# Optimization experiments

Hardware: AMD Instinct MI355X
Metric: run time of the kernel (lower is better)

The kernel has to match this reference:

```python
import jax, jax.numpy as jnp
import numpy as np

NDIM = 1024
NHEAD = 16
HEAD_DIM = NDIM // NHEAD


def setup_inputs() -> dict:
    key = jax.random.key(0)
    ks = jax.random.split(key, 12)
    B, L, C = 2, 2048, NDIM
    s = 0.02
    return {
        "q": jax.random.normal(ks[0], (B, L, C), jnp.float32),
        "k": jax.random.normal(ks[1], (B, L, C), jnp.float32),
        "v": jax.random.normal(ks[2], (B, L, C), jnp.float32),
        "Wq": jax.random.normal(ks[3], (C, C), jnp.float32) * s,
        "bq": jax.random.normal(ks[4], (C,), jnp.float32) * s,
        "Wk": jax.random.normal(ks[5], (C, C), jnp.float32) * s,
        "bk": jax.random.normal(ks[6], (C,), jnp.float32) * s,
        "Wv": jax.random.normal(ks[7], (C, C), jnp.float32) * s,
        "bv": jax.random.normal(ks[8], (C,), jnp.float32) * s,
        "Wo": jax.random.normal(ks[9], (C, C), jnp.float32) * s,
        "bo": jax.random.normal(ks[10], (C,), jnp.float32) * s,
    }


def reference(q, k, v, Wq, bq, Wk, bk, Wv, bv, Wo, bo):
    B, Lq, C = q.shape
    H, D = NHEAD, HEAD_DIM
    # projections, then split heads: (B, H, L, D)
    qh = (q @ Wq + bq).reshape(B, Lq, H, D).transpose(0, 2, 1, 3)
    kh = (k @ Wk + bk).reshape(B, k.shape[1], H, D).transpose(0, 2, 1, 3)
    vh = (v @ Wv + bv).reshape(B, v.shape[1], H, D).transpose(0, 2, 1, 3)
    scale = 1.0 / jnp.sqrt(jnp.asarray(D, qh.dtype))
    att = jnp.einsum("bhqd,bhkd->bhqk", qh, kh) * scale  # (B,H,Lq,Lk)
    att = jax.nn.softmax(att, axis=-1)  # dropout p=0.0 -> identity
    y = jnp.einsum("bhqk,bhkd->bhqd", att, vh)
    y = y.transpose(0, 2, 1, 3).reshape(B, Lq, C)
    return y @ Wo + bo
```

## Files before the change

kernel.cpp:

```cpp
#include <hip/hip_runtime.h>
#include <math.h>

#define BATCH 2
#define SEQ   2048
#define CDIM  1024
#define NHEAD 16
#define HDIM  64
#define TOKS  (BATCH * SEQ)

typedef __bf16 bf16x8 __attribute__((ext_vector_type(8)));
typedef __bf16 bf16x2 __attribute__((ext_vector_type(2)));
typedef float  f32x4  __attribute__((ext_vector_type(4)));
typedef float  f32x16 __attribute__((ext_vector_type(16)));

#define MFMA16(a, b, c) __builtin_amdgcn_mfma_f32_16x16x32_bf16(a, b, c, 0, 0, 0)
#define MFMA32(a, b, c) __builtin_amdgcn_mfma_f32_32x32x16_bf16(a, b, c, 0, 0, 0)

#define QSCALE 0.1803368801111204f

__device__ __forceinline__ void gload_lds16(const __bf16* g, __bf16* l) {
    __builtin_amdgcn_global_load_lds(
        (const __attribute__((address_space(1))) unsigned int*)g,
        (__attribute__((address_space(3))) unsigned int*)l, 16, 0, 0);
}

__global__ __launch_bounds__(256) void prep_kernel(
    const float* __restrict__ q, const float* __restrict__ k, const float* __restrict__ v,
    __bf16* __restrict__ qo, __bf16* __restrict__ ko, __bf16* __restrict__ vo,
    const float* __restrict__ W0, const float* __restrict__ W1,
    const float* __restrict__ W2, const float* __restrict__ W3,
    __bf16* __restrict__ T0, __bf16* __restrict__ T1,
    __bf16* __restrict__ T2, __bf16* __restrict__ T3)
{
    __shared__ __bf16 Ts[64][72];
    const int bx = blockIdx.x;
    const int tid = threadIdx.x;

    if (bx < 6144) {
        const int t = bx >> 11;
        const size_t i = ((size_t)(bx & 2047) * 256 + tid) * 8;
        const float* s = t == 0 ? q : (t == 1 ? k : v);
        __bf16* d = t == 0 ? qo : (t == 1 ? ko : vo);
        const float4 x = *(const float4*)&s[i];
        const float4 y = *(const float4*)&s[i + 4];
        bf16x8 o;
        o[0] = (__bf16)x.x; o[1] = (__bf16)x.y; o[2] = (__bf16)x.z; o[3] = (__bf16)x.w;
        o[4] = (__bf16)y.x; o[5] = (__bf16)y.y; o[6] = (__bf16)y.z; o[7] = (__bf16)y.w;
        *(bf16x8*)&d[i] = o;
        return;
    }

    const int t  = bx - 6144;
    const int z  = t >> 8;
    const int ry = (t & 255) >> 4;
    const int rx = t & 15;
    const float* W = z == 0 ? W0 : z == 1 ? W1 : z == 2 ? W2 : W3;
    __bf16* T = z == 0 ? T0 : z == 1 ? T1 : z == 2 ? T2 : T3;
    const int rb = ry * 64, cb = rx * 64;
    const int r = tid >> 4;
    const int c4 = (tid & 15) * 4;
#pragma unroll
    for (int p = 0; p < 4; p++) {
        const int rr = p * 16 + r;
        const float4 w4 = *(const float4*)&W[(size_t)(rb + rr) * CDIM + cb + c4];
        Ts[c4 + 0][rr] = (__bf16)w4.x;
        Ts[c4 + 1][rr] = (__bf16)w4.y;
        Ts[c4 + 2][rr] = (__bf16)w4.z;
        Ts[c4 + 3][rr] = (__bf16)w4.w;
    }
    __syncthreads();
    const int n = tid >> 2;
    const int k16 = (tid & 3) * 16;
    *(bf16x8*)&T[(size_t)(cb + n) * CDIM + rb + k16]     = *(const bf16x8*)&Ts[n][k16];
    *(bf16x8*)&T[(size_t)(cb + n) * CDIM + rb + k16 + 8] = *(const bf16x8*)&Ts[n][k16 + 8];
}

__global__ __launch_bounds__(512, 6) void qkv_gemm_kernel(
    const __bf16* __restrict__ qb, const __bf16* __restrict__ kb,
    const __bf16* __restrict__ vb,
    const __bf16* __restrict__ Wqt, const __bf16* __restrict__ Wkt,
    const __bf16* __restrict__ Wvt,
    const float* __restrict__ bq, const float* __restrict__ bk,
    const float* __restrict__ bv,
    __bf16* __restrict__ Qh, __bf16* __restrict__ Kh, __bf16* __restrict__ Vht)
{
    __shared__ __bf16 As[2][128 * 32];
    __shared__ __bf16 Bs[2][128 * 32];

    const int lin = blockIdx.x + (blockIdx.y << 3) + (blockIdx.z << 8);
    const int nl  = (lin & 7) * 96 + (lin >> 3);
    const int bx  = nl & 7;
    const int by  = (nl >> 3) & 31;
    const int z   = nl >> 8;

    const __bf16* A    = z == 0 ? qb : z == 1 ? kb : Wvt;
    const __bf16* Bt   = z == 0 ? Wqt : z == 1 ? Wkt : vb;
    const float*  bias = z == 0 ? bq : z == 1 ? bk : bv;

    const int tid  = threadIdx.x;
    const int w    = tid >> 6;
    const int lane = tid & 63;
    const int quad = lane >> 4;
    const int c    = lane & 15;
    const int wm   = w >> 1;
    const int wn   = w & 1;
    const int rowBase = (z == 2 ? bx : by) * 128;
    const int colBase = (z == 2 ? by : bx) * 128;

    const int sr = lane >> 2;
    const int sk = (lane & 3) * 8;

    f32x4 acc[2][4];
#pragma unroll
    for (int i = 0; i < 2; i++)
#pragma unroll
        for (int j = 0; j < 4; j++) acc[i][j] = (f32x4){0, 0, 0, 0};

    const __bf16* srcA = A  + (size_t)(rowBase + w * 16 + sr) * CDIM + sk;
    const __bf16* srcB = Bt + (size_t)(colBase + w * 16 + sr) * CDIM + sk;
    const int dstOff = w * 16 * 32;

#define QSTAGE(K0, BB)                                   \
    {                                                    \
        gload_lds16(srcA + (K0), &As[BB][dstOff]);       \
        gload_lds16(srcB + (K0), &Bs[BB][dstOff]);       \
    }

    QSTAGE(0, 0);
    __syncthreads();

    int buf = 0;
    for (int k0 = 0; k0 < CDIM; k0 += 32) {
        if (k0 + 32 < CDIM) {
            if (buf == 0) QSTAGE(k0 + 32, 1) else QSTAGE(k0 + 32, 0)
        }

        bf16x8 af[2], bf[4];
#pragma unroll
        for (int i = 0; i < 2; i++)
            af[i] = *(const bf16x8*)&As[buf][(wm * 32 + i * 16 + c) * 32 + quad * 8];
#pragma unroll
        for (int i = 0; i < 4; i++)
            bf[i] = *(const bf16x8*)&Bs[buf][(wn * 64 + i * 16 + c) * 32 + quad * 8];
#pragma unroll
        for (int mi = 0; mi < 2; mi++)
#pragma unroll
            for (int ni = 0; ni < 4; ni++)
                acc[mi][ni] = MFMA16(af[mi], bf[ni], acc[mi][ni]);
        __syncthreads();
        buf ^= 1;
    }
#undef QSTAGE

#pragma unroll
    for (int mi = 0; mi < 2; mi++) {
#pragma unroll
        for (int ni = 0; ni < 4; ni++) {
            const int col = colBase + wn * 64 + ni * 16 + c;
#pragma unroll
            for (int r = 0; r < 4; r++) {
                const int row = rowBase + wm * 32 + mi * 16 + quad * 4 + r;
                const float val = acc[mi][ni][r];
                if (z == 2) {
                    Vht[(size_t)row * TOKS + col] = (__bf16)(val + bias[row]);
                } else {
                    const int b = row >> 11, l = row & 2047;
                    const int h = col >> 6,  d = col & 63;
                    const float s = (z == 0) ? QSCALE : 1.0f;
                    __bf16* outp = (z == 0) ? Qh : Kh;
                    outp[((((size_t)b * NHEAD + h) * SEQ) + l) * HDIM + d] =
                        (__bf16)((val + bias[col]) * s);
                }
            }
        }
    }
}

__global__ __launch_bounds__(512, 4) void out_gemm_kernel(
    const __bf16* __restrict__ A, const __bf16* __restrict__ Bt,
    const float* __restrict__ bias, float* __restrict__ out)
{
    __shared__ __bf16 As[2][128 * 32];
    __shared__ __bf16 Bs[2][64 * 32];

    const int lin = blockIdx.x + (blockIdx.y << 4);
    const int nl  = (lin & 7) * 64 + (lin >> 3);
    const int bx  = nl & 15;
    const int by  = nl >> 4;

    const int tid  = threadIdx.x;
    const int w    = tid >> 6;
    const int lane = tid & 63;
    const int quad = lane >> 4;
    const int c    = lane & 15;
    const int wm   = w >> 1;
    const int wn   = w & 1;
    const int rowBase = by * 128;
    const int colBase = bx * 64;
    const int sr = lane >> 2;
    const int sk = (lane & 3) * 8;

    f32x4 acc[2][2];
#pragma unroll
    for (int i = 0; i < 2; i++)
#pragma unroll
        for (int j = 0; j < 2; j++) acc[i][j] = (f32x4){0, 0, 0, 0};

    const __bf16* srcA = A + (size_t)(rowBase + w * 16 + sr) * CDIM + sk;
    const __bf16* srcB = Bt + (size_t)(colBase + (w & 3) * 16 + sr) * CDIM + sk;
    const int dstAoff = w * 16 * 32;
    const int dstBoff = (w & 3) * 16 * 32;

#define OSTAGE(K0, BB)                                           \
    {                                                            \
        gload_lds16(srcA + (K0), &As[BB][dstAoff]);              \
        if (w < 4) gload_lds16(srcB + (K0), &Bs[BB][dstBoff]);   \
    }

    OSTAGE(0, 0);
    __syncthreads();

    int buf = 0;
    for (int k0 = 0; k0 < CDIM; k0 += 32) {
        if (k0 + 32 < CDIM) {
            if (buf == 0) OSTAGE(k0 + 32, 1) else OSTAGE(k0 + 32, 0)
        }

        bf16x8 af[2], bf[2];
#pragma unroll
        for (int i = 0; i < 2; i++)
            af[i] = *(const bf16x8*)&As[buf][(wm * 32 + i * 16 + c) * 32 + quad * 8];
#pragma unroll
        for (int i = 0; i < 2; i++)
            bf[i] = *(const bf16x8*)&Bs[buf][(wn * 32 + i * 16 + c) * 32 + quad * 8];
#pragma unroll
        for (int mi = 0; mi < 2; mi++)
#pragma unroll
            for (int ni = 0; ni < 2; ni++)
                acc[mi][ni] = MFMA16(af[mi], bf[ni], acc[mi][ni]);
        __syncthreads();
        buf ^= 1;
    }
#undef OSTAGE

#pragma unroll
    for (int mi = 0; mi < 2; mi++) {
#pragma unroll
        for (int ni = 0; ni < 2; ni++) {
            const int col = colBase + wn * 32 + ni * 16 + c;
#pragma unroll
            for (int r = 0; r < 4; r++) {
                const int row = rowBase + wm * 32 + mi * 16 + quad * 4 + r;
                out[(size_t)row * CDIM + col] = acc[mi][ni][r] + bias[col];
            }
        }
    }
}

__global__ __launch_bounds__(256, 2) void attn_v13_kernel(
    const __bf16* __restrict__ Qh, const __bf16* __restrict__ Kh,
    const __bf16* __restrict__ Vht, __bf16* __restrict__ Y)
{
    __shared__ __align__(16) __bf16 lds[2][2][2][8 * 520];

    const int tid  = threadIdx.x;
    const int w    = tid >> 6;
    const int wq   = w & 1;
    const int kh   = w >> 1;
    const int lane = tid & 63;
    const int l31  = lane & 31;
    const int hi   = lane >> 5;
    const int rr8  = l31 & 7;
    const int cb   = (l31 >> 3) * 520 + rr8 * 64;
    const int bh   = blockIdx.x;
    const int b    = bh >> 4;
    const int h    = bh & 15;
    const int qbase = blockIdx.y * 128 + wq * 64;

    const __bf16* Qg  = Qh + (size_t)bh * SEQ * HDIM;
    const __bf16* KgB = Kh + (size_t)bh * SEQ * HDIM;
    const __bf16* VgB = Vht + (size_t)(h * HDIM) * TOKS + (size_t)b * SEQ;

    bf16x8 qf0[4], qf1[4];
#pragma unroll
    for (int ks = 0; ks < 4; ks++) {
        qf0[ks] = *(const bf16x8*)&Qg[(size_t)(qbase + l31) * HDIM + ks * 16 + hi * 8];
        qf1[ks] = *(const bf16x8*)&Qg[(size_t)(qbase + 32 + l31) * HDIM + ks * 16 + hi * 8];
    }

    f32x16 O00, O01, O10, O11;
#pragma unroll
    for (int j = 0; j < 16; j++) {
        O00[j] = 0.0f; O01[j] = 0.0f; O10[j] = 0.0f; O11[j] = 0.0f;
    }
    float Lp0 = 0.0f, Lp1 = 0.0f;

    const int sidx = w & 1;
    const int iskv = w >> 1;
    const int kr8 = lane >> 3, kc = lane & 7;

#define STAGE(T, bb)                                                          \
    {                                                                         \
        _Pragma("unroll")                                                     \
        for (int jj = 0; jj < 8; jj++) {                                      \
            if (iskv == 0)                                                    \
                gload_lds16(KgB + (size_t)(sidx * 1024 + (T) + 8 * jj + kr8) * HDIM \
                                + ((kc ^ kr8) * 8),                           \
                            &lds[bb][sidx][0][jj * 520]);                     \
            else                                                              \
                gload_lds16(VgB + (size_t)(8 * jj + kr8) * TOKS               \
                                + sidx * 1024 + (T) + ((kc ^ kr8) * 8),       \
                            &lds[bb][sidx][1][jj * 520]);                     \
        }                                                                     \
    }

#define PACK_AF(P, KL, AF)                                                    \
    {                                                                         \
        const int r0 = (KL) * 8;                                              \
        union { bf16x2 v; unsigned int u; } pa, pb, pc, pd;                   \
        pa.v[0] = (__bf16)P[r0 + 0]; pa.v[1] = (__bf16)P[r0 + 1];             \
        pb.v[0] = (__bf16)P[r0 + 2]; pb.v[1] = (__bf16)P[r0 + 3];             \
        pc.v[0] = (__bf16)P[r0 + 4]; pc.v[1] = (__bf16)P[r0 + 5];             \
        pd.v[0] = (__bf16)P[r0 + 6]; pd.v[1] = (__bf16)P[r0 + 7];             \
        asm volatile("v_permlane32_swap_b32 %0, %1" : "+v"(pa.u), "+v"(pc.u)); \
        asm volatile("v_permlane32_swap_b32 %0, %1" : "+v"(pb.u), "+v"(pd.u)); \
        AF.u[0] = pa.u; AF.u[1] = pb.u; AF.u[2] = pc.u; AF.u[3] = pd.u;       \
    }

    STAGE(0, 0);
    __syncthreads();

    int buf = 0;
    for (int t0 = 0; t0 < 1024; t0 += 64) {
        const int tn = t0 + 64;
        if (tn < 1024) {
            if (buf == 0) STAGE(tn, 1) else STAGE(tn, 0)
        }

        const __bf16* ldsK = &lds[buf][kh][0][0];
        const __bf16* ldsV = &lds[buf][kh][1][0];

#pragma unroll
        for (int kt = 0; kt < 2; kt++) {
            const bf16x8 kf0 = *(const bf16x8*)&ldsK[kt * 2080 + cb + (((0 + hi) ^ rr8) * 8)];
            const bf16x8 kf1 = *(const bf16x8*)&ldsK[kt * 2080 + cb + (((2 + hi) ^ rr8) * 8)];
            const bf16x8 kf2 = *(const bf16x8*)&ldsK[kt * 2080 + cb + (((4 + hi) ^ rr8) * 8)];
            const bf16x8 kf3 = *(const bf16x8*)&ldsK[kt * 2080 + cb + (((6 + hi) ^ rr8) * 8)];

            f32x16 s0, s1;
#pragma unroll
            for (int j = 0; j < 16; j++) { s0[j] = 0.0f; s1[j] = 0.0f; }
            s0 = MFMA32(kf0, qf0[0], s0);
            s1 = MFMA32(kf0, qf1[0], s1);
            s0 = MFMA32(kf1, qf0[1], s0);
            s1 = MFMA32(kf1, qf1[1], s1);
            s0 = MFMA32(kf2, qf0[2], s0);
            s1 = MFMA32(kf2, qf1[2], s1);
            s0 = MFMA32(kf3, qf0[3], s0);
            s1 = MFMA32(kf3, qf1[3], s1);

            float p0[16], p1[16];
#pragma unroll
            for (int j = 0; j < 16; j++) {
                p0[j] = __builtin_amdgcn_exp2f(s0[j]);
                p1[j] = __builtin_amdgcn_exp2f(s1[j]);
            }
#pragma unroll
            for (int j = 0; j < 16; j++) {
                Lp0 += p0[j];
                Lp1 += p1[j];
            }

#pragma unroll
            for (int kl = 0; kl < 2; kl++) {
                union AFU { unsigned int u[4]; bf16x8 v; } af0, af1;
                PACK_AF(p0, kl, af0);
                PACK_AF(p1, kl, af1);
                const int sv = (((kt * 4 + kl * 2 + hi) ^ rr8) * 8);
                const bf16x8 vf0 = *(const bf16x8*)&ldsV[cb + sv];
                const bf16x8 vf1 = *(const bf16x8*)&ldsV[2080 + cb + sv];
                __builtin_amdgcn_s_setprio(1);
                O00 = MFMA32(af0.v, vf0, O00);
                O01 = MFMA32(af0.v, vf1, O01);
                O10 = MFMA32(af1.v, vf0, O10);
                O11 = MFMA32(af1.v, vf1, O11);
                __builtin_amdgcn_s_setprio(0);
            }
        }

        __syncthreads();
        buf ^= 1;
    }
#undef STAGE

    float* scr  = (float*)&lds[0][0][0][0];
    float* scrL = scr + 8192;
    const int wl = wq * 64 + lane;

#define SPILL(OP, OPI)                                                        \
    { union { f32x16 v; f32x4 q[4]; } tt; tt.v = OP;                          \
      _Pragma("unroll")                                                       \
      for (int part = 0; part < 4; part++)                                    \
          *(f32x4*)&scr[(((OPI) * 4 + part) * 128 + wl) * 4] = tt.q[part]; }

#define MERGE(OP, OPI)                                                        \
    { union { f32x16 v; f32x4 q[4]; } tt; tt.v = OP;                          \
      _Pragma("unroll")                                                       \
      for (int part = 0; part < 4; part++)                                    \
          tt.q[part] += *(const f32x4*)&scr[(((OPI) * 4 + part) * 128 + wl) * 4]; \
      OP = tt.v; }

    if (kh == 1) {
        SPILL(O00, 0); SPILL(O01, 1); SPILL(O10, 2); SPILL(O11, 3);
        scrL[wl]       = Lp0;
        scrL[128 + wl] = Lp1;
    }
    __syncthreads();
    if (kh == 0) {
        MERGE(O00, 0); MERGE(O01, 1); MERGE(O10, 2); MERGE(O11, 3);
        Lp0 += scrL[wl];
        Lp1 += scrL[128 + wl];

        const float Lt0 = Lp0 + __shfl_xor(Lp0, 32);
        const float Lt1 = Lp1 + __shfl_xor(Lp1, 32);
        const float inv0 = 1.0f / Lt0;
        const float inv1 = 1.0f / Lt1;

        __bf16* Yb = Y + (size_t)b * SEQ * CDIM;
#pragma unroll
        for (int reg = 0; reg < 16; reg++) {
            const int qrow = (reg & 3) + 8 * (reg >> 2) + 4 * hi;
            const float i0 = __shfl(inv0, qrow);
            const float i1 = __shfl(inv1, qrow);
            __bf16* yp0 = Yb + (size_t)(qbase + qrow) * CDIM + h * HDIM + l31;
            __bf16* yp1 = Yb + (size_t)(qbase + 32 + qrow) * CDIM + h * HDIM + l31;
            yp0[0]  = (__bf16)(O00[reg] * i0);
            yp0[32] = (__bf16)(O01[reg] * i0);
            yp1[0]  = (__bf16)(O10[reg] * i1);
            yp1[32] = (__bf16)(O11[reg] * i1);
        }
    }
#undef SPILL
#undef MERGE
#undef PACK_AF
}


extern "C" void kernel_launch(void* const* d_in, const int* in_sizes, int n_in,
                              void* d_out, int out_size, void* d_ws, size_t ws_size,
                              hipStream_t stream)
{
    const float* q  = (const float*)d_in[0];
    const float* k  = (const float*)d_in[1];
    const float* v  = (const float*)d_in[2];
    const float* Wq = (const float*)d_in[3];
    const float* bq = (const float*)d_in[4];
    const float* Wk = (const float*)d_in[5];
    const float* bk = (const float*)d_in[6];
    const float* Wv = (const float*)d_in[7];
    const float* bv = (const float*)d_in[8];
    const float* Wo = (const float*)d_in[9];
    const float* bo = (const float*)d_in[10];
    float* out = (float*)d_out;

    const size_t MAT = (size_t)TOKS * CDIM;
    const size_t WN  = (size_t)CDIM * CDIM;

    __bf16* p   = (__bf16*)d_ws;
    __bf16* qb  = p; p += MAT;
    __bf16* kb  = p; p += MAT;
    __bf16* vb  = p; p += MAT;
    __bf16* Wqt = p; p += WN;
    __bf16* Wkt = p; p += WN;
    __bf16* Wvt = p; p += WN;
    __bf16* Wot = p; p += WN;
    __bf16* Qh  = p; p += MAT;
    __bf16* Kh  = p; p += MAT;
    __bf16* Vht = p; p += MAT;
    __bf16* Yb  = qb;

    prep_kernel<<<dim3(7168), dim3(256), 0, stream>>>(
        q, k, v, qb, kb, vb, Wq, Wk, Wv, Wo, Wqt, Wkt, Wvt, Wot);

    qkv_gemm_kernel<<<dim3(8, 32, 3), dim3(512), 0, stream>>>(
        qb, kb, vb, Wqt, Wkt, Wvt, bq, bk, bv, Qh, Kh, Vht);

    attn_v13_kernel<<<dim3(BATCH * NHEAD, SEQ / 128), dim3(256), 0, stream>>>(Qh, Kh, Vht, Yb);

    out_gemm_kernel<<<dim3(16, 32), dim3(512), 0, stream>>>(Yb, Wot, bo, out);
}
```

Baseline: 214.7 us.

## Fuse fp32-to-bf16 activation conversion into QKV GEMM tile loading

```diff
diff --git a/kernel.cpp b/kernel.cpp
--- a/kernel.cpp
+++ b/kernel.cpp
@@ -25,32 +25,14 @@
 }
 
 __global__ __launch_bounds__(256) void prep_kernel(
-    const float* __restrict__ q, const float* __restrict__ k, const float* __restrict__ v,
-    __bf16* __restrict__ qo, __bf16* __restrict__ ko, __bf16* __restrict__ vo,
     const float* __restrict__ W0, const float* __restrict__ W1,
     const float* __restrict__ W2, const float* __restrict__ W3,
     __bf16* __restrict__ T0, __bf16* __restrict__ T1,
     __bf16* __restrict__ T2, __bf16* __restrict__ T3)
 {
     __shared__ __bf16 Ts[64][72];
-    const int bx = blockIdx.x;
+    const int t  = blockIdx.x;
     const int tid = threadIdx.x;
-
-    if (bx < 6144) {
-        const int t = bx >> 11;
-        const size_t i = ((size_t)(bx & 2047) * 256 + tid) * 8;
-        const float* s = t == 0 ? q : (t == 1 ? k : v);
-        __bf16* d = t == 0 ? qo : (t == 1 ? ko : vo);
-        const float4 x = *(const float4*)&s[i];
-        const float4 y = *(const float4*)&s[i + 4];
-        bf16x8 o;
-        o[0] = (__bf16)x.x; o[1] = (__bf16)x.y; o[2] = (__bf16)x.z; o[3] = (__bf16)x.w;
-        o[4] = (__bf16)y.x; o[5] = (__bf16)y.y; o[6] = (__bf16)y.z; o[7] = (__bf16)y.w;
-        *(bf16x8*)&d[i] = o;
-        return;
-    }
-
-    const int t  = bx - 6144;
     const int z  = t >> 8;
     const int ry = (t & 255) >> 4;
     const int rx = t & 15;
@@ -76,8 +58,8 @@
 }
 
 __global__ __launch_bounds__(512, 6) void qkv_gemm_kernel(
-    const __bf16* __restrict__ qb, const __bf16* __restrict__ kb,
-    const __bf16* __restrict__ vb,
+    const float* __restrict__ qf, const float* __restrict__ kf,
+    const float* __restrict__ vf,
     const __bf16* __restrict__ Wqt, const __bf16* __restrict__ Wkt,
     const __bf16* __restrict__ Wvt,
     const float* __restrict__ bq, const float* __restrict__ bk,
@@ -93,8 +75,8 @@
     const int by  = (nl >> 3) & 31;
     const int z   = nl >> 8;
 
-    const __bf16* A    = z == 0 ? qb : z == 1 ? kb : Wvt;
-    const __bf16* Bt   = z == 0 ? Wqt : z == 1 ? Wkt : vb;
+    const float*  F    = z == 0 ? qf : z == 1 ? kf : vf;
+    const __bf16* Wm   = z == 0 ? Wqt : z == 1 ? Wkt : Wvt;
     const float*  bias = z == 0 ? bq : z == 1 ? bk : bv;
 
     const int tid  = threadIdx.x;
@@ -106,6 +88,8 @@
     const int wn   = w & 1;
     const int rowBase = (z == 2 ? bx : by) * 128;
     const int colBase = (z == 2 ? by : bx) * 128;
+    const int tokBase = (z == 2) ? colBase : rowBase;
+    const int wBase   = (z == 2) ? rowBase : colBase;
 
     const int sr = lane >> 2;
     const int sk = (lane & 3) * 8;
@@ -116,41 +100,60 @@
 #pragma unroll
         for (int j = 0; j < 4; j++) acc[i][j] = (f32x4){0, 0, 0, 0};
 
-    const __bf16* srcA = A  + (size_t)(rowBase + w * 16 + sr) * CDIM + sk;
-    const __bf16* srcB = Bt + (size_t)(colBase + w * 16 + sr) * CDIM + sk;
+    const float*  srcF = F  + (size_t)(tokBase + w * 16 + sr) * CDIM + sk;
+    const __bf16* srcW = Wm + (size_t)(wBase   + w * 16 + sr) * CDIM + sk;
+    __bf16* ldsTok = (z == 2) ? &Bs[0][0] : &As[0][0];
+    __bf16* ldsW   = (z == 2) ? &As[0][0] : &Bs[0][0];
     const int dstOff = w * 16 * 32;
-
-#define QSTAGE(K0, BB)                                   \
-    {                                                    \
-        gload_lds16(srcA + (K0), &As[BB][dstOff]);       \
-        gload_lds16(srcB + (K0), &Bs[BB][dstOff]);       \
-    }
-
-    QSTAGE(0, 0);
+    const int dstWr  = dstOff + lane * 8;
+
+#define CVT8(FA, FB, O)                                                       \
+    { O[0] = (__bf16)FA.x; O[1] = (__bf16)FA.y; O[2] = (__bf16)FA.z;          \
+      O[3] = (__bf16)FA.w; O[4] = (__bf16)FB.x; O[5] = (__bf16)FB.y;          \
+      O[6] = (__bf16)FB.z; O[7] = (__bf16)FB.w; }
+
+    {
+        gload_lds16(srcW, ldsW + dstOff);
+        const float4 fa = *(const float4*)&srcF[0];
+        const float4 fb = *(const float4*)&srcF[4];
+        bf16x8 o;
+        CVT8(fa, fb, o)
+        *(bf16x8*)(ldsTok + dstWr) = o;
+    }
     __syncthreads();
 
     int buf = 0;
     for (int k0 = 0; k0 < CDIM; k0 += 32) {
-        if (k0 + 32 < CDIM) {
-            if (buf == 0) QSTAGE(k0 + 32, 1) else QSTAGE(k0 + 32, 0)
-        }
-
-        bf16x8 af[2], bf[4];
+        const bool pre = (k0 + 32 < CDIM);
+        float4 fa, fb;
+        if (pre) {
+            gload_lds16(srcW + k0 + 32, ldsW + (buf ^ 1) * 4096 + dstOff);
+            fa = *(const float4*)&srcF[k0 + 32];
+            fb = *(const float4*)&srcF[k0 + 36];
+        }
+
+        bf16x8 af[2], bff[4];
 #pragma unroll
         for (int i = 0; i < 2; i++)
             af[i] = *(const bf16x8*)&As[buf][(wm * 32 + i * 16 + c) * 32 + quad * 8];
 #pragma unroll
         for (int i = 0; i < 4; i++)
-            bf[i] = *(const bf16x8*)&Bs[buf][(wn * 64 + i * 16 + c) * 32 + quad * 8];
+            bff[i] = *(const bf16x8*)&Bs[buf][(wn * 64 + i * 16 + c) * 32 + quad * 8];
 #pragma unroll
         for (int mi = 0; mi < 2; mi++)
 #pragma unroll
             for (int ni = 0; ni < 4; ni++)
-                acc[mi][ni] = MFMA16(af[mi], bf[ni], acc[mi][ni]);
+                acc[mi][ni] = MFMA16(af[mi], bff[ni], acc[mi][ni]);
+
+        if (pre) {
+            bf16x8 o;
+            CVT8(fa, fb, o)
+            *(bf16x8*)(ldsTok + (buf ^ 1) * 4096 + dstWr) = o;
+        }
         __syncthreads();
         buf ^= 1;
     }
-#undef QSTAGE
+#undef CVT8
 
 #pragma unroll
     for (int mi = 0; mi < 2; mi++) {
@@ -467,9 +470,6 @@
     const size_t WN  = (size_t)CDIM * CDIM;
 
     __bf16* p   = (__bf16*)d_ws;
-    __bf16* qb  = p; p += MAT;
-    __bf16* kb  = p; p += MAT;
-    __bf16* vb  = p; p += MAT;
     __bf16* Wqt = p; p += WN;
     __bf16* Wkt = p; p += WN;
     __bf16* Wvt = p; p += WN;
@@ -477,13 +477,13 @@
     __bf16* Qh  = p; p += MAT;
     __bf16* Kh  = p; p += MAT;
     __bf16* Vht = p; p += MAT;
-    __bf16* Yb  = qb;
-
-    prep_kernel<<<dim3(7168), dim3(256), 0, stream>>>(
-        q, k, v, qb, kb, vb, Wq, Wk, Wv, Wo, Wqt, Wkt, Wvt, Wot);
+    __bf16* Yb  = p; p += MAT;
+
+    prep_kernel<<<dim3(1024), dim3(256), 0, stream>>>(
+        Wq, Wk, Wv, Wo, Wqt, Wkt, Wvt, Wot);
 
     qkv_gemm_kernel<<<dim3(8, 32, 3), dim3(512), 0, stream>>>(
-        qb, kb, vb, Wqt, Wkt, Wvt, bq, bk, bv, Qh, Kh, Vht);
+        q, k, v, Wqt, Wkt, Wvt, bq, bk, bv, Qh, Kh, Vht);
 
     attn_v13_kernel<<<dim3(BATCH * NHEAD, SEQ / 128), dim3(256), 0, stream>>>(Qh, Kh, Vht, Yb);
 
```

Result: slower. 227.0 us (+5.7%).
